# Kernel tuning notes

Hardware: AMD Instinct MI355X
Metric: run time of the kernel (lower is better)

Reference implementation:

```python
import jax, jax.numpy as jnp
import numpy as np

EPS = 1e-5

def _ln(x):
    m = jnp.mean(x, axis=-1, keepdims=True)
    v = jnp.mean((x - m) ** 2, axis=-1, keepdims=True)
    return (x - m) / jnp.sqrt(v + EPS)

def setup_inputs() -> dict:
    key = jax.random.key(0)
    ks = jax.random.split(key, 6)
    B, S, E, H = 2, 2048, 1024, 16
    sd = 1.0 / np.sqrt(E)
    x = jax.random.normal(ks[0], (B, S, E), dtype=jnp.float32)
    w_in = jax.random.normal(ks[1], (3 * E, E), dtype=jnp.float32) * sd
    w_out = jax.random.normal(ks[2], (E, E), dtype=jnp.float32) * sd
    w_fc = jax.random.normal(ks[3], (4 * E, E), dtype=jnp.float32) * sd
    b_fc = jnp.zeros((4 * E,), dtype=jnp.float32)
    w_proj = jax.random.normal(ks[4], (E, 4 * E), dtype=jnp.float32) * (1.0 / np.sqrt(4 * E))
    b_proj = jnp.zeros((E,), dtype=jnp.float32)
    return {"x": x, "w_in": w_in, "w_out": w_out, "w_fc": w_fc,
            "b_fc": b_fc, "w_proj": w_proj, "b_proj": b_proj}

def reference(x, w_in, w_out, w_fc, b_fc, w_proj, b_proj):
    B, S, E = x.shape
    H = 16
    D = E // H
    h = _ln(x)
    qkv = h @ w_in.T                      # [B,S,3E]
    q, k, v = jnp.split(qkv, 3, axis=-1)
    q = q.reshape(B, S, H, D)
    k = k.reshape(B, S, H, D)
    v = v.reshape(B, S, H, D)
    scale = 1.0 / np.sqrt(D)
    scores = jnp.einsum('bqhd,bkhd->bhqk', q, k) * scale  # [B,H,S,S]
    causal = jnp.tril(jnp.ones((S, S), dtype=bool))
    scores = jnp.where(causal, scores, -jnp.inf)
    attn = jax.nn.softmax(scores, axis=-1)
    o = jnp.einsum('bhqk,bkhd->bqhd', attn, v).reshape(B, S, E)
    attn_out = o @ w_out.T
    x2 = x + attn_out                      # residual 1
    h2 = _ln(x2)
    m = jax.nn.relu(h2 @ w_fc.T + b_fc)    # [B,S,4E]
    return (m @ w_proj.T + b_proj) + x2    # residual 2
```

## Files before the change

### kernel.cpp

```cpp
#include <hip/hip_runtime.h>
#include <stdint.h>

#define AS1 __attribute__((address_space(1)))
#define AS3 __attribute__((address_space(3)))

typedef __bf16 bf8_t __attribute__((ext_vector_type(8)));
typedef float f4_t __attribute__((ext_vector_type(4)));
typedef unsigned short ush;

__device__ __forceinline__ ush f2b(float f) {
  unsigned u = __builtin_bit_cast(unsigned, f);
  u += 0x7fffu + ((u >> 16) & 1u);
  return (ush)(u >> 16);
}
__device__ __forceinline__ void unpack8(uint4 u, float* dst) {
  unsigned a0 = u.x, a1 = u.y, a2 = u.z, a3 = u.w;
  dst[0] = __builtin_bit_cast(float, a0 << 16);
  dst[1] = __builtin_bit_cast(float, a0 & 0xffff0000u);
  dst[2] = __builtin_bit_cast(float, a1 << 16);
  dst[3] = __builtin_bit_cast(float, a1 & 0xffff0000u);
  dst[4] = __builtin_bit_cast(float, a2 << 16);
  dst[5] = __builtin_bit_cast(float, a2 & 0xffff0000u);
  dst[6] = __builtin_bit_cast(float, a3 << 16);
  dst[7] = __builtin_bit_cast(float, a3 & 0xffff0000u);
}

__global__ __launch_bounds__(256) void f2b_all(
    const float* __restrict__ w_in, const float* __restrict__ w_out,
    const float* __restrict__ w_fc, const float* __restrict__ w_proj,
    ush* __restrict__ o_in, ush* __restrict__ o_out,
    ush* __restrict__ o_fc, ush* __restrict__ o_proj) {
  const int blk = blockIdx.x;
  const float* src;
  ush* dst;
  int base;
  if (blk < 3072) { src = w_in; dst = o_in; base = blk; }
  else if (blk < 4096) { src = w_out; dst = o_out; base = blk - 3072; }
  else if (blk < 8192) { src = w_fc; dst = o_fc; base = blk - 4096; }
  else { src = w_proj; dst = o_proj; base = blk - 8192; }
  const int i = (base * 256 + threadIdx.x) * 4;
  float4 v = *(const float4*)(src + i);
  union { ush u[4]; uint2 d; } p;
  p.u[0] = f2b(v.x); p.u[1] = f2b(v.y); p.u[2] = f2b(v.z); p.u[3] = f2b(v.w);
  *(uint2*)(dst + i) = p.d;
}

__global__ __launch_bounds__(256) void ln_kernel(const float* __restrict__ x,
                                                 ush* __restrict__ out) {
  const int row = blockIdx.x, tid = threadIdx.x;
  const float* xr = x + (size_t)row * 1024;
  float4 v = ((const float4*)xr)[tid];
  float s = v.x + v.y + v.z + v.w;
  float q = v.x * v.x + v.y * v.y + v.z * v.z + v.w * v.w;
  for (int o = 32; o; o >>= 1) { s += __shfl_down(s, o); q += __shfl_down(q, o); }
  __shared__ float rs[4], rq[4];
  const int w = tid >> 6;
  if ((tid & 63) == 0) { rs[w] = s; rq[w] = q; }
  __syncthreads();
  s = rs[0] + rs[1] + rs[2] + rs[3];
  q = rq[0] + rq[1] + rq[2] + rq[3];
  const float mean = s * (1.0f / 1024.0f);
  const float var = q * (1.0f / 1024.0f) - mean * mean;
  const float rstd = rsqrtf(var + 1e-5f);
  union { ush u[4]; uint2 d; } p;
  p.u[0] = f2b((v.x - mean) * rstd);
  p.u[1] = f2b((v.y - mean) * rstd);
  p.u[2] = f2b((v.z - mean) * rstd);
  p.u[3] = f2b((v.w - mean) * rstd);
  *(uint2*)(out + (size_t)row * 1024 + tid * 4) = p.d;
}

template <int EPI>
__global__ __launch_bounds__(512, 2) void gemm8p(
    const ush* __restrict__ A, const ush* __restrict__ Bw,
    int M, int N, int K, int lda, int ldb,
    const float* __restrict__ bias, const float* __restrict__ resid,
    float* __restrict__ outF, ush* __restrict__ outB) {
  __shared__ __align__(16) ush lds[65536];
  ush* const LA0 = lds;
  ush* const LA1 = lds + 16384;
  ush* const LB0 = lds + 32768;
  ush* const LB1 = lds + 49152;

  const int tid = threadIdx.x;
  const int wave = tid >> 6, lane = tid & 63;
  const int wm = wave >> 2, wn = wave & 3;
  const int l16 = lane & 15, quad = lane >> 4;
  const int sw = l16 & 7;
  const int bm = blockIdx.x, bn = blockIdx.y;
  const int bmrow = bm * 256, bnrow = bn * 256;
  const size_t kbase = (size_t)blockIdx.z * (size_t)K;
  const int KT = K >> 6;
  const int nit = KT >> 1;
  const int gcs = (((lane & 7) ^ ((lane >> 3) & 7)) << 3);

  auto stage = [&](const ush* __restrict__ gbase, int blkrow, int ld,
                   ush* dstbase, int t, int h) {
    const int kt = t & (KT - 1);
#pragma unroll
    for (int i2 = 0; i2 < 2; ++i2) {
      const int rr = h * 128 + (wave * 2 + i2) * 8 + (lane >> 3);
      const ush* g = gbase + (size_t)(blkrow + rr) * ld + kbase + kt * 64 + gcs;
      __builtin_amdgcn_global_load_lds(
          (const AS1 void*)g,
          (AS3 void*)(dstbase + h * 8192 + (wave * 2 + i2) * 512), 16, 0, 0);
    }
  };

  f4_t acc[8][4];
#pragma unroll
  for (int i = 0; i < 8; ++i)
#pragma unroll
    for (int j = 0; j < 4; ++j) acc[i][j] = (f4_t){0.f, 0.f, 0.f, 0.f};

  stage(A, bmrow, lda, LA0, 0, 0);
  stage(A, bmrow, lda, LA0, 0, 1);
  stage(Bw, bnrow, ldb, LB0, 0, 0);
  stage(Bw, bnrow, ldb, LB0, 0, 1);
  stage(A, bmrow, lda, LA1, 1, 0);
  asm volatile("s_waitcnt vmcnt(2)" ::: "memory");
  __builtin_amdgcn_s_barrier();

  bf8_t af[4][2], bf[2][2];

  for (int it = 0; it < nit; ++it) {
#pragma unroll
    for (int hf = 0; hf < 2; ++hf) {
      ush* const cA = hf ? LA1 : LA0;
      ush* const cB = hf ? LB1 : LB0;
#pragma unroll
      for (int sub = 0; sub < 4; ++sub) {
        const int p = hf * 4 + sub;
        if (sub == 0) {
#pragma unroll
          for (int m = 0; m < 4; ++m)
#pragma unroll
            for (int kk = 0; kk < 2; ++kk)
              af[m][kk] = *(const bf8_t*)&cA[(wm * 128 + m * 16 + l16) * 64 +
                                            (((kk * 4 + quad) ^ sw) << 3)];
#pragma unroll
          for (int n = 0; n < 2; ++n)
#pragma unroll
            for (int kk = 0; kk < 2; ++kk)
              bf[n][kk] = *(const bf8_t*)&cB[(wn * 64 + n * 16 + l16) * 64 +
                                            (((kk * 4 + quad) ^ sw) << 3)];
        } else if (sub == 1) {
#pragma unroll
          for (int n = 0; n < 2; ++n)
#pragma unroll
            for (int kk = 0; kk < 2; ++kk)
              bf[n][kk] = *(const bf8_t*)&cB[(wn * 64 + (2 + n) * 16 + l16) * 64 +
                                            (((kk * 4 + quad) ^ sw) << 3)];
        } else if (sub == 2) {
#pragma unroll
          for (int m = 0; m < 4; ++m)
#pragma unroll
            for (int kk = 0; kk < 2; ++kk)
              af[m][kk] = *(const bf8_t*)&cA[(wm * 128 + (4 + m) * 16 + l16) * 64 +
                                            (((kk * 4 + quad) ^ sw) << 3)];
#pragma unroll
          for (int n = 0; n < 2; ++n)
#pragma unroll
            for (int kk = 0; kk < 2; ++kk)
              bf[n][kk] = *(const bf8_t*)&cB[(wn * 64 + n * 16 + l16) * 64 +
                                            (((kk * 4 + quad) ^ sw) << 3)];
        } else {
#pragma unroll
          for (int n = 0; n < 2; ++n)
#pragma unroll
            for (int kk = 0; kk < 2; ++kk)
              bf[n][kk] = *(const bf8_t*)&cB[(wn * 64 + (2 + n) * 16 + l16) * 64 +
                                            (((kk * 4 + quad) ^ sw) << 3)];
        }
        if (p == 0) stage(A, bmrow, lda, LA1, 2 * it + 1, 1);
        else if (p == 1) stage(Bw, bnrow, ldb, LB1, 2 * it + 1, 0);
        else if (p == 2) stage(Bw, bnrow, ldb, LB1, 2 * it + 1, 1);
        else if (p == 3) stage(A, bmrow, lda, LA0, 2 * it + 2, 0);
        else if (p == 4) stage(A, bmrow, lda, LA0, 2 * it + 2, 1);
        else if (p == 5) stage(Bw, bnrow, ldb, LB0, 2 * it + 2, 0);
        else if (p == 6) stage(Bw, bnrow, ldb, LB0, 2 * it + 2, 1);
        else stage(A, bmrow, lda, LA1, 2 * it + 3, 0);
        if (sub == 3) asm volatile("s_waitcnt vmcnt(2)" ::: "memory");
        __builtin_amdgcn_s_barrier();
        asm volatile("s_waitcnt lgkmcnt(0)" ::: "memory");
        __builtin_amdgcn_sched_barrier(0);
        __builtin_amdgcn_s_setprio(1);
        const int mo = (sub >= 2) ? 4 : 0;
        const int no = (sub & 1) ? 2 : 0;
#pragma unroll
        for (int m = 0; m < 4; ++m)
#pragma unroll
          for (int n = 0; n < 2; ++n)
#pragma unroll
            for (int kk = 0; kk < 2; ++kk)
              acc[mo + m][no + n] = __builtin_amdgcn_mfma_f32_16x16x32_bf16(
                  af[m][kk], bf[n][kk], acc[mo + m][no + n], 0, 0, 0);
        __builtin_amdgcn_s_setprio(0);
        __builtin_amdgcn_s_barrier();
      }
    }
  }

  asm volatile("s_waitcnt vmcnt(0)" ::: "memory");
  __builtin_amdgcn_s_barrier();

  if (EPI == 0 || EPI == 2) {
    ush* outBz = outB + (size_t)blockIdx.z * ((size_t)M * N);
    ush* eb = lds + wave * 8192;
    float bv[4];
    if (EPI == 2) {
#pragma unroll
      for (int ni = 0; ni < 4; ++ni) bv[ni] = bias[bn * 256 + wn * 64 + ni * 16 + l16];
    }
#pragma unroll
    for (int mi = 0; mi < 8; ++mi)
#pragma unroll
      for (int ni = 0; ni < 4; ++ni)
#pragma unroll
        for (int r = 0; r < 4; ++r) {
          float v = acc[mi][ni][r];
          if (EPI == 2) v = fmaxf(v + bv[ni], 0.0f);
          eb[(mi * 16 + quad * 4 + r) * 64 + ni * 16 + l16] = f2b(v);
        }
    asm volatile("s_waitcnt lgkmcnt(0)" ::: "memory");
#pragma unroll
    for (int j = 0; j < 16; ++j) {
      const int lr = j * 8 + (lane >> 3);
      const int c8 = (lane & 7) * 8;
      uint4 v = *(const uint4*)&eb[lr * 64 + c8];
      *(uint4*)(outBz + (size_t)(bm * 256 + wm * 128 + lr) * N + bn * 256 +
                wn * 64 + c8) = v;
    }
  } else {
#pragma unroll
    for (int mi = 0; mi < 8; ++mi)
#pragma unroll
      for (int ni = 0; ni < 4; ++ni) {
        const int gm0 = bm * 256 + wm * 128 + mi * 16 + quad * 4;
        const int gn = bn * 256 + wn * 64 + ni * 16 + l16;
        const float bv = (EPI == 3) ? bias[gn] : 0.0f;
#pragma unroll
        for (int r = 0; r < 4; ++r) {
          const size_t idx = (size_t)(gm0 + r) * N + gn;
          outF[idx] = acc[mi][ni][r] + bv + resid[idx];
        }
      }
  }
}

__global__ __launch_bounds__(256) void reduce4(const ush* __restrict__ p,
                                               const float* __restrict__ bias,
                                               const float* __restrict__ resid,
                                               float* __restrict__ out) {
  const size_t i = ((size_t)blockIdx.x * 256 + threadIdx.x) * 8;
  const int col = (int)(i & 1023);
  float acc[8];
  float4 r0 = *(const float4*)(resid + i);
  float4 r1 = *(const float4*)(resid + i + 4);
  acc[0] = r0.x + bias[col + 0]; acc[1] = r0.y + bias[col + 1];
  acc[2] = r0.z + bias[col + 2]; acc[3] = r0.w + bias[col + 3];
  acc[4] = r1.x + bias[col + 4]; acc[5] = r1.y + bias[col + 5];
  acc[6] = r1.z + bias[col + 6]; acc[7] = r1.w + bias[col + 7];
#pragma unroll
  for (int z = 0; z < 4; ++z) {
    uint4 u = *(const uint4*)(p + (size_t)z * 4194304 + i);
    float f[8]; unpack8(u, f);
#pragma unroll
    for (int j = 0; j < 8; ++j) acc[j] += f[j];
  }
  *(float4*)(out + i) = *(float4*)acc;
  *(float4*)(out + i + 4) = *(float4*)(acc + 4);
}

template <int EPI, int BM, int MINW>
__global__ __launch_bounds__(256, MINW) void gemm_bt(
    const ush* __restrict__ A, const ush* __restrict__ Bw,
    int M, int N, int K,
    const float* __restrict__ bias, const float* __restrict__ resid,
    float* __restrict__ outF, ush* __restrict__ outB) {
  constexpr int MI = BM / 32;
  constexpr int NCH = (BM + 128) / 16;
  constexpr int PC = NCH / 4;
  constexpr int ASZ = BM * 32;
  __shared__ ush lds[2 * ASZ + 2 * 4096];
  const int tid = threadIdx.x;
  const int wave = tid >> 6, lane = tid & 63;
  const int bm = blockIdx.x, bn = blockIdx.y;
  const int wm = (wave & 1) * (BM / 2), wn = (wave >> 1) * 64;
  const int l16 = lane & 15, quad = lane >> 4;
  const int srow = lane >> 2;
  const int scol = (lane & 3) * 8;

  const ush* Abase = A + (size_t)(bm * BM) * K;
  const ush* Bbase = Bw + (size_t)(bn * 128) * K;

  f4_t acc[MI][4];
#pragma unroll
  for (int i = 0; i < MI; ++i)
#pragma unroll
    for (int j = 0; j < 4; ++j) acc[i][j] = (f4_t){0.f, 0.f, 0.f, 0.f};

  const int kiters = K >> 5;

  auto stage = [&](int k0, int buf) {
    const int kk = k0 * 32;
#pragma unroll
    for (int i = 0; i < PC; ++i) {
      const int c = wave * PC + i;
      if (c < BM / 16) {
        const ush* ga = Abase + (size_t)(c * 16 + srow) * K + kk + scol;
        __builtin_amdgcn_global_load_lds((const AS1 void*)ga,
                                         (AS3 void*)(lds + buf * ASZ + c * 512), 16, 0, 0);
      } else {
        const int c2 = c - BM / 16;
        const ush* gb = Bbase + (size_t)(c2 * 16 + srow) * K + kk + scol;
        __builtin_amdgcn_global_load_lds(
            (const AS1 void*)gb, (AS3 void*)(lds + 2 * ASZ + buf * 4096 + c2 * 512), 16, 0, 0);
      }
    }
  };

  stage(0, 0);
  __syncthreads();
  for (int k0 = 0; k0 < kiters; ++k0) {
    const int cur = k0 & 1;
    if (k0 + 1 < kiters) stage(k0 + 1, cur ^ 1);
    bf8_t af[MI], bfr[4];
#pragma unroll
    for (int mi = 0; mi < MI; ++mi)
      af[mi] = *(const bf8_t*)&lds[cur * ASZ + (wm + mi * 16 + l16) * 32 + quad * 8];
#pragma unroll
    for (int ni = 0; ni < 4; ++ni)
      bfr[ni] = *(const bf8_t*)&lds[2 * ASZ + cur * 4096 + (wn + ni * 16 + l16) * 32 + quad * 8];
#pragma unroll
    for (int mi = 0; mi < MI; ++mi)
#pragma unroll
      for (int ni = 0; ni < 4; ++ni)
        acc[mi][ni] =
            __builtin_amdgcn_mfma_f32_16x16x32_bf16(af[mi], bfr[ni], acc[mi][ni], 0, 0, 0);
    __syncthreads();
  }

  if (EPI == 0 || EPI == 2) {
    ush* eb = lds + wave * ASZ;
#pragma unroll
    for (int mi = 0; mi < MI; ++mi)
#pragma unroll
      for (int ni = 0; ni < 4; ++ni) {
        const int gn = bn * 128 + wn + ni * 16 + l16;
        const float bv = (EPI == 2) ? bias[gn] : 0.0f;
#pragma unroll
        for (int r = 0; r < 4; ++r) {
          float v = acc[mi][ni][r] + bv;
          if (EPI == 2) v = fmaxf(v, 0.0f);
          eb[(mi * 16 + quad * 4 + r) * 64 + ni * 16 + l16] = f2b(v);
        }
      }
#pragma unroll
    for (int j = 0; j < BM / 16; ++j) {
      const int lr = j * 8 + (lane >> 3);
      const int c8 = (lane & 7) * 8;
      uint4 v = *(const uint4*)&eb[lr * 64 + c8];
      *(uint4*)(outB + (size_t)(bm * BM + wm + lr) * N + bn * 128 + wn + c8) = v;
    }
  } else {
#pragma unroll
    for (int mi = 0; mi < MI; ++mi) {
#pragma unroll
      for (int ni = 0; ni < 4; ++ni) {
        const int gm0 = bm * BM + wm + mi * 16 + quad * 4;
        const int gn = bn * 128 + wn + ni * 16 + l16;
        const float bv = (EPI == 3) ? bias[gn] : 0.0f;
#pragma unroll
        for (int r = 0; r < 4; ++r) {
          const size_t idx = (size_t)(gm0 + r) * N + gn;
          outF[idx] = acc[mi][ni][r] + bv + resid[idx];
        }
      }
    }
  }
}

__global__ __launch_bounds__(256) void pack_kv(const ush* __restrict__ qkv,
                                               ush* __restrict__ Kp,
                                               ush* __restrict__ Vp) {
  const int lin = blockIdx.x;
  const int kt = lin & 31, h = (lin >> 5) & 15, b = lin >> 9;
  const int tid = threadIdx.x;
  __shared__ ush Vs[64 * 72];
  const size_t rowbase = (size_t)(b * 2048 + kt * 64) * 3072 + h * 64;
  ush* Kt = Kp + (size_t)lin * 4096;
  ush* Vt = Vp + (size_t)lin * 4096;

  const int r0 = tid >> 3, cin = tid & 7;
#pragma unroll
  for (int it = 0; it < 2; ++it) {
    const int r = r0 + it * 32;
    uint4 ku = *(const uint4*)(qkv + rowbase + (size_t)r * 3072 + 1024 + cin * 8);
    float f[8]; unpack8(ku, f);
    union { ush us[8]; uint4 v; } pk;
#pragma unroll
    for (int j = 0; j < 8; ++j) pk.us[j] = f2b(f[j] * 0.18033688f);
    *(uint4*)(Kt + (size_t)(r * 8 + (cin ^ (r & 7))) * 8) = pk.v;
    uint4 vu = *(const uint4*)(qkv + rowbase + (size_t)r * 3072 + 2048 + cin * 8);
    *(uint4*)&Vs[r * 72 + cin * 8] = vu;
  }
  __syncthreads();
#pragma unroll
  for (int oc2 = 0; oc2 < 2; ++oc2) {
    const int oc = tid * 2 + oc2;
    const int d = oc >> 3, c = oc & 7;
    const int k0 = 8 * (c ^ (d & 7));
    union { ush us[8]; uint4 v; } pk;
#pragma unroll
    for (int j = 0; j < 8; ++j) pk.us[j] = Vs[(k0 + j) * 72 + d];
    *(uint4*)(Vt + (size_t)oc * 8) = pk.v;
  }
}

__global__ __launch_bounds__(256, 4) void attn_kernel(const ush* __restrict__ qkv,
                                                      const ush* __restrict__ Kp,
                                                      const ush* __restrict__ Vp,
                                                      ush* __restrict__ o) {
  const int lin = blockIdx.x;
  const int b = lin & 1, h = (lin >> 1) & 15;
  const int sg = lin >> 5, jg = sg >> 3, kg = sg & 7;
  const int tq = (jg == 0) ? (31 - 2 * kg)
               : (jg == 1) ? (2 * kg)
               : (jg == 2) ? (30 - 2 * kg)
                           : (2 * kg + 1);
  const int tid = threadIdx.x;
  const int wave = tid >> 6, lane = tid & 63;
  const int l15 = lane & 15, quad = lane >> 4;

  __shared__ __align__(16) ush Ks[2 * 4096];
  __shared__ __align__(16) ush Vt[2 * 4096];
  __shared__ __align__(16) ush Ps[64 * 64];

  bf8_t qf[2];
  {
    const int qrow = b * 2048 + tq * 64 + wave * 16 + l15;
#pragma unroll
    for (int s = 0; s < 2; ++s) {
      union { uint4 u; bf8_t v; } pk;
      pk.u = *(const uint4*)(qkv + (size_t)qrow * 3072 + h * 64 + s * 32 + quad * 8);
      qf[s] = pk.v;
    }
  }

  float m_s = -1e30f, l_part = 0.f;
  f4_t O[4];
#pragma unroll
  for (int j = 0; j < 4; ++j) O[j] = (f4_t){0.f, 0.f, 0.f, 0.f};

  const int qw0 = tq * 64 + wave * 16;
  const int swz = (l15 & 7) * 8;
  const int prow = wave * 16 + l15;
  const int pswz = (prow & 7) << 3;
  const size_t tile0 = (size_t)((b * 16 + h) * 32) * 4096;

  {
    const ush* Ktile = Kp + tile0;
    const ush* Vtile = Vp + tile0;
#pragma unroll
    for (int i = 0; i < 2; ++i) {
      const int seg = wave * 2 + i;
      __builtin_amdgcn_global_load_lds((const AS1 void*)(Ktile + seg * 512 + lane * 8),
                                       (AS3 void*)(Ks + seg * 512), 16, 0, 0);
      __builtin_amdgcn_global_load_lds((const AS1 void*)(Vtile + seg * 512 + lane * 8),
                                       (AS3 void*)(Vt + seg * 512), 16, 0, 0);
    }
  }
  asm volatile("s_waitcnt vmcnt(0)" ::: "memory");
  __builtin_amdgcn_s_barrier();

  for (int kt = 0; kt <= tq; ++kt) {
    const int cur = (kt & 1) * 4096;
    const int nxt = 4096 - cur;
    if (kt < tq) {
      const ush* Ktile = Kp + tile0 + (size_t)(kt + 1) * 4096;
      const ush* Vtile = Vp + tile0 + (size_t)(kt + 1) * 4096;
#pragma unroll
      for (int i = 0; i < 2; ++i) {
        const int seg = wave * 2 + i;
        __builtin_amdgcn_global_load_lds((const AS1 void*)(Ktile + seg * 512 + lane * 8),
                                         (AS3 void*)(Ks + nxt + seg * 512), 16, 0, 0);
        __builtin_amdgcn_global_load_lds((const AS1 void*)(Vtile + seg * 512 + lane * 8),
                                         (AS3 void*)(Vt + nxt + seg * 512), 16, 0, 0);
      }
    }

    bf8_t vf[4][2];
#pragma unroll
    for (int n4 = 0; n4 < 4; ++n4)
#pragma unroll
      for (int s = 0; s < 2; ++s)
        vf[n4][s] = *(const bf8_t*)&Vt[cur + (n4 * 16 + l15) * 64 + (((4 * s + quad) * 8) ^ swz)];

    f4_t S[4];
#pragma unroll
    for (int mi = 0; mi < 4; ++mi) S[mi] = (f4_t){0.f, 0.f, 0.f, 0.f};
    __builtin_amdgcn_s_setprio(1);
#pragma unroll
    for (int s = 0; s < 2; ++s)
#pragma unroll
      for (int mi = 0; mi < 4; ++mi) {
        bf8_t kf = *(const bf8_t*)&Ks[cur + (mi * 16 + l15) * 64 + (((4 * s + quad) * 8) ^ swz)];
        S[mi] = __builtin_amdgcn_mfma_f32_16x16x32_bf16(kf, qf[s], S[mi], 0, 0, 0);
      }
    __builtin_amdgcn_s_setprio(0);

    if (kt == tq) {
#pragma unroll
      for (int mi = 0; mi < 4; ++mi)
#pragma unroll
        for (int r = 0; r < 4; ++r) {
          const int kg2 = kt * 64 + mi * 16 + quad * 4 + r;
          const int qg = qw0 + l15;
          if (kg2 > qg) S[mi][r] = -1e30f;
        }
    }

    float t0 = fmaxf(fmaxf(S[0][0], S[0][1]), fmaxf(S[0][2], S[0][3]));
    float t1 = fmaxf(fmaxf(S[1][0], S[1][1]), fmaxf(S[1][2], S[1][3]));
    float t2 = fmaxf(fmaxf(S[2][0], S[2][1]), fmaxf(S[2][2], S[2][3]));
    float t3 = fmaxf(fmaxf(S[3][0], S[3][1]), fmaxf(S[3][2], S[3][3]));
    float mx = fmaxf(fmaxf(t0, t1), fmaxf(t2, t3));
    mx = fmaxf(mx, __shfl_xor(mx, 16));
    mx = fmaxf(mx, __shfl_xor(mx, 32));

    if (!__all(mx - m_s <= 8.0f)) {
      const float mn = fmaxf(m_s, mx);
      const float dm = m_s - mn;
      float alpha;
      asm("v_exp_f32 %0, %1" : "=v"(alpha) : "v"(dm));
      float ar[4];
#pragma unroll
      for (int r = 0; r < 4; ++r) ar[r] = __shfl(alpha, quad * 4 + r);
#pragma unroll
      for (int n4 = 0; n4 < 4; ++n4)
#pragma unroll
        for (int r = 0; r < 4; ++r) O[n4][r] *= ar[r];
      l_part *= alpha;
      m_s = mn;
    }

    float sum = 0.f;
#pragma unroll
    for (int mi = 0; mi < 4; ++mi)
#pragma unroll
      for (int r = 0; r < 4; ++r) {
        const float z = S[mi][r] - m_s;
        float pv;
        asm("v_exp_f32 %0, %1" : "=v"(pv) : "v"(z));
        S[mi][r] = pv;
        sum += pv;
      }
    l_part += sum;

#pragma unroll
    for (int mi = 0; mi < 4; ++mi) {
      uint2 w2;
      asm("v_cvt_pk_bf16_f32 %0, %1, %2" : "=v"(w2.x) : "v"(S[mi][0]), "v"(S[mi][1]));
      asm("v_cvt_pk_bf16_f32 %0, %1, %2" : "=v"(w2.y) : "v"(S[mi][2]), "v"(S[mi][3]));
      *(uint2*)&Ps[prow * 64 + ((mi * 16 + quad * 4) ^ pswz)] = w2;
    }

    bf8_t pf[2];
#pragma unroll
    for (int s = 0; s < 2; ++s)
      pf[s] = *(const bf8_t*)&Ps[prow * 64 + ((s * 32 + quad * 8) ^ pswz)];
    __builtin_amdgcn_s_setprio(1);
#pragma unroll
    for (int n4 = 0; n4 < 4; ++n4)
#pragma unroll
      for (int s = 0; s < 2; ++s)
        O[n4] = __builtin_amdgcn_mfma_f32_16x16x32_bf16(pf[s], vf[n4][s], O[n4], 0, 0, 0);
    __builtin_amdgcn_s_setprio(0);

    asm volatile("s_waitcnt vmcnt(0)" ::: "memory");
    __builtin_amdgcn_s_barrier();
  }

  float l_s = l_part;
  l_s += __shfl_xor(l_s, 16);
  l_s += __shfl_xor(l_s, 32);
  const float rc = 1.0f / l_s;
  float rr[4];
#pragma unroll
  for (int r = 0; r < 4; ++r) rr[r] = __shfl(rc, quad * 4 + r);
#pragma unroll
  for (int n4 = 0; n4 < 4; ++n4)
#pragma unroll
    for (int r = 0; r < 4; ++r) {
      const int qg = tq * 64 + wave * 16 + quad * 4 + r;
      o[(size_t)(b * 2048 + qg) * 1024 + h * 64 + n4 * 16 + l15] = f2b(O[n4][r] * rr[r]);
    }
}

extern "C" void kernel_launch(void* const* d_in, const int* in_sizes, int n_in,
                              void* d_out, int out_size, void* d_ws, size_t ws_size,
                              hipStream_t stream) {
  const float* x = (const float*)d_in[0];
  const float* w_in = (const float*)d_in[1];
  const float* w_out = (const float*)d_in[2];
  const float* w_fc = (const float*)d_in[3];
  const float* b_fc = (const float*)d_in[4];
  const float* w_proj = (const float*)d_in[5];
  const float* b_proj = (const float*)d_in[6];
  float* out = (float*)d_out;

  char* ws = (char*)d_ws;
  ush* w_in_b = (ush*)(ws);
  ush* w_out_b = (ush*)(ws + 6291456);
  ush* h_b = (ush*)(ws + 8388608);
  ush* Kp = (ush*)(ws + 16777216);
  ush* Vp = (ush*)(ws + 25165824);
  ush* Pp = (ush*)(ws);
  ush* w_fc_b = (ush*)(ws + 33554432);
  ush* w_proj_b = (ush*)(ws + 41943040);
  float* x2 = (float*)(ws + 50331648);
  ush* qkv_b = (ush*)(ws + 67108864);
  ush* m_b = (ush*)(ws + 67108864);
  ush* o_b = (ush*)(ws + 92274688);

  f2b_all<<<12288, 256, 0, stream>>>(w_in, w_out, w_fc, w_proj,
                                     w_in_b, w_out_b, w_fc_b, w_proj_b);

  ln_kernel<<<4096, 256, 0, stream>>>(x, h_b);

  gemm8p<0><<<dim3(16, 12), 512, 0, stream>>>(
      h_b, w_in_b, 4096, 3072, 1024, 1024, 1024, nullptr, nullptr, nullptr, qkv_b);

  pack_kv<<<1024, 256, 0, stream>>>(qkv_b, Kp, Vp);

  attn_kernel<<<1024, 256, 0, stream>>>(qkv_b, Kp, Vp, o_b);

  gemm_bt<1, 64, 4><<<dim3(64, 8), 256, 0, stream>>>(
      o_b, w_out_b, 4096, 1024, 1024, nullptr, x, x2, nullptr);

  ln_kernel<<<4096, 256, 0, stream>>>(x2, h_b);

  gemm8p<2><<<dim3(16, 16), 512, 0, stream>>>(
      h_b, w_fc_b, 4096, 4096, 1024, 1024, 1024, b_fc, nullptr, nullptr, m_b);

  gemm8p<0><<<dim3(16, 4, 4), 512, 0, stream>>>(
      m_b, w_proj_b, 4096, 1024, 1024, 4096, 4096, nullptr, nullptr, nullptr, Pp);

  reduce4<<<2048, 256, 0, stream>>>(Pp, b_proj, x2, out);
}
```

Baseline: 298.4 us.

## Fuse weight cast with first layernorm; register-staged K/V prefetch in attention

Merges the weight bf16-cast kernel and the first layernorm into one launch by giving the extra blocks layernorm rows, which removes one kernel launch and its tail. In the attention kernel, K/V tile prefetch moves from direct global-to-LDS loads to loads into registers issued two tiles ahead. Those registers are written to the other LDS buffer one iteration later, and the per-iteration wait now covers LDS traffic rather than vector-memory traffic, so global latency is hidden across a whole iteration. This costs extra VGPRs, which could lower occupancy, and adds explicit LDS stores.

```diff
diff --git a/kernel.cpp b/kernel.cpp
--- a/kernel.cpp
+++ b/kernel.cpp
@@ -25,29 +25,8 @@
   dst[7] = __builtin_bit_cast(float, a3 & 0xffff0000u);
 }
 
-__global__ __launch_bounds__(256) void f2b_all(
-    const float* __restrict__ w_in, const float* __restrict__ w_out,
-    const float* __restrict__ w_fc, const float* __restrict__ w_proj,
-    ush* __restrict__ o_in, ush* __restrict__ o_out,
-    ush* __restrict__ o_fc, ush* __restrict__ o_proj) {
-  const int blk = blockIdx.x;
-  const float* src;
-  ush* dst;
-  int base;
-  if (blk < 3072) { src = w_in; dst = o_in; base = blk; }
-  else if (blk < 4096) { src = w_out; dst = o_out; base = blk - 3072; }
-  else if (blk < 8192) { src = w_fc; dst = o_fc; base = blk - 4096; }
-  else { src = w_proj; dst = o_proj; base = blk - 8192; }
-  const int i = (base * 256 + threadIdx.x) * 4;
-  float4 v = *(const float4*)(src + i);
-  union { ush u[4]; uint2 d; } p;
-  p.u[0] = f2b(v.x); p.u[1] = f2b(v.y); p.u[2] = f2b(v.z); p.u[3] = f2b(v.w);
-  *(uint2*)(dst + i) = p.d;
-}
-
-__global__ __launch_bounds__(256) void ln_kernel(const float* __restrict__ x,
-                                                 ush* __restrict__ out) {
-  const int row = blockIdx.x, tid = threadIdx.x;
+__device__ __forceinline__ void ln_row(const float* __restrict__ x,
+                                       ush* __restrict__ out, int row, int tid) {
   const float* xr = x + (size_t)row * 1024;
   float4 v = ((const float4*)xr)[tid];
   float s = v.x + v.y + v.z + v.w;
@@ -70,6 +49,36 @@
   *(uint2*)(out + (size_t)row * 1024 + tid * 4) = p.d;
 }
 
+__global__ __launch_bounds__(256) void f2b_ln(
+    const float* __restrict__ w_in, const float* __restrict__ w_out,
+    const float* __restrict__ w_fc, const float* __restrict__ w_proj,
+    ush* __restrict__ o_in, ush* __restrict__ o_out,
+    ush* __restrict__ o_fc, ush* __restrict__ o_proj,
+    const float* __restrict__ x, ush* __restrict__ h_b) {
+  const int blk = blockIdx.x;
+  if (blk >= 12288) {
+    ln_row(x, h_b, blk - 12288, threadIdx.x);
+    return;
+  }
+  const float* src;
+  ush* dst;
+  int base;
+  if (blk < 3072) { src = w_in; dst = o_in; base = blk; }
+  else if (blk < 4096) { src = w_out; dst = o_out; base = blk - 3072; }
+  else if (blk < 8192) { src = w_fc; dst = o_fc; base = blk - 4096; }
+  else { src = w_proj; dst = o_proj; base = blk - 8192; }
+  const int i = (base * 256 + threadIdx.x) * 4;
+  float4 v = *(const float4*)(src + i);
+  union { ush u[4]; uint2 d; } p;
+  p.u[0] = f2b(v.x); p.u[1] = f2b(v.y); p.u[2] = f2b(v.z); p.u[3] = f2b(v.w);
+  *(uint2*)(dst + i) = p.d;
+}
+
+__global__ __launch_bounds__(256) void ln_kernel(const float* __restrict__ x,
+                                                 ush* __restrict__ out) {
+  ln_row(x, out, blockIdx.x, threadIdx.x);
+}
+
 template <int EPI>
 __global__ __launch_bounds__(512, 2) void gemm8p(
     const ush* __restrict__ A, const ush* __restrict__ Bw,
@@ -458,35 +467,34 @@
   const int prow = wave * 16 + l15;
   const int pswz = (prow & 7) << 3;
   const size_t tile0 = (size_t)((b * 16 + h) * 32) * 4096;
-
-  {
-    const ush* Ktile = Kp + tile0;
-    const ush* Vtile = Vp + tile0;
-#pragma unroll
-    for (int i = 0; i < 2; ++i) {
-      const int seg = wave * 2 + i;
-      __builtin_amdgcn_global_load_lds((const AS1 void*)(Ktile + seg * 512 + lane * 8),
-                                       (AS3 void*)(Ks + seg * 512), 16, 0, 0);
-      __builtin_amdgcn_global_load_lds((const AS1 void*)(Vtile + seg * 512 + lane * 8),
-                                       (AS3 void*)(Vt + seg * 512), 16, 0, 0);
-    }
-  }
-  asm volatile("s_waitcnt vmcnt(0)" ::: "memory");
+  const ush* const KT0 = Kp + tile0;
+  const ush* const VT0 = Vp + tile0;
+  const int sA = (wave * 2 + 0) * 512 + lane * 8;
+  const int sB = (wave * 2 + 1) * 512 + lane * 8;
+
+  uint4 ka, kb, va, vb;
+  ka = *(const uint4*)(KT0 + sA); kb = *(const uint4*)(KT0 + sB);
+  va = *(const uint4*)(VT0 + sA); vb = *(const uint4*)(VT0 + sB);
+  *(uint4*)(Ks + sA) = ka; *(uint4*)(Ks + sB) = kb;
+  *(uint4*)(Vt + sA) = va; *(uint4*)(Vt + sB) = vb;
+  if (tq >= 1) {
+    ka = *(const uint4*)(KT0 + 4096 + sA); kb = *(const uint4*)(KT0 + 4096 + sB);
+    va = *(const uint4*)(VT0 + 4096 + sA); vb = *(const uint4*)(VT0 + 4096 + sB);
+  }
+  asm volatile("s_waitcnt lgkmcnt(0)" ::: "memory");
   __builtin_amdgcn_s_barrier();
 
   for (int kt = 0; kt <= tq; ++kt) {
     const int cur = (kt & 1) * 4096;
     const int nxt = 4096 - cur;
-    if (kt < tq) {
-      const ush* Ktile = Kp + tile0 + (size_t)(kt + 1) * 4096;
-      const ush* Vtile = Vp + tile0 + (size_t)(kt + 1) * 4096;
-#pragma unroll
-      for (int i = 0; i < 2; ++i) {
-        const int seg = wave * 2 + i;
-        __builtin_amdgcn_global_load_lds((const AS1 void*)(Ktile + seg * 512 + lane * 8),
-                                         (AS3 void*)(Ks + nxt + seg * 512), 16, 0, 0);
-        __builtin_amdgcn_global_load_lds((const AS1 void*)(Vtile + seg * 512 + lane * 8),
-                                         (AS3 void*)(Vt + nxt + seg * 512), 16, 0, 0);
+    if (kt + 1 <= tq) {
+      *(uint4*)(Ks + nxt + sA) = ka; *(uint4*)(Ks + nxt + sB) = kb;
+      *(uint4*)(Vt + nxt + sA) = va; *(uint4*)(Vt + nxt + sB) = vb;
+      if (kt + 2 <= tq) {
+        const ush* K2 = KT0 + (size_t)(kt + 2) * 4096;
+        const ush* V2 = VT0 + (size_t)(kt + 2) * 4096;
+        ka = *(const uint4*)(K2 + sA); kb = *(const uint4*)(K2 + sB);
+        va = *(const uint4*)(V2 + sA); vb = *(const uint4*)(V2 + sB);
       }
     }
 
@@ -578,7 +586,7 @@
         O[n4] = __builtin_amdgcn_mfma_f32_16x16x32_bf16(pf[s], vf[n4][s], O[n4], 0, 0, 0);
     __builtin_amdgcn_s_setprio(0);
 
-    asm volatile("s_waitcnt vmcnt(0)" ::: "memory");
+    asm volatile("s_waitcnt lgkmcnt(0)" ::: "memory");
     __builtin_amdgcn_s_barrier();
   }
 
@@ -624,10 +632,8 @@
   ush* m_b = (ush*)(ws + 67108864);
   ush* o_b = (ush*)(ws + 92274688);
 
-  f2b_all<<<12288, 256, 0, stream>>>(w_in, w_out, w_fc, w_proj,
-                                     w_in_b, w_out_b, w_fc_b, w_proj_b);
-
-  ln_kernel<<<4096, 256, 0, stream>>>(x, h_b);
+  f2b_ln<<<16384, 256, 0, stream>>>(w_in, w_out, w_fc, w_proj,
+                                    w_in_b, w_out_b, w_fc_b, w_proj_b, x, h_b);
 
   gemm8p<0><<<dim3(16, 12), 512, 0, stream>>>(
       h_b, w_in_b, 4096, 3072, 1024, 1024, 1024, nullptr, nullptr, nullptr, qkv_b);
```

After: 294.9 us. Within noise of the previous version (-1.2%).
